# Kernel optimization log

Measured on AMD Instinct MI355X. Metric: run time of the kernel, lower is better.

## Reference

```python
import jax, jax.numpy as jnp
import numpy as np

DIM = 256
HEADS = 8
WS = 8
HID = 512
EPS = 1e-5

def _rel_index(ws):
    coords = np.arange(ws)
    grid = np.stack(np.meshgrid(coords, coords, indexing='ij')).reshape(2, -1)
    rel = (grid[:, :, None] - grid[:, None, :]).transpose(1, 2, 0)
    rel[:, :, 0] += ws - 1
    rel[:, :, 1] += ws - 1
    rel[:, :, 0] *= 2 * ws - 1
    return jnp.asarray(rel.sum(-1))  # [ws*ws, ws*ws] int

REL = _rel_index(WS)

def setup_inputs():
    key = jax.random.key(0)
    ks = iter(jax.random.split(key, 64))
    def w(shape, scale=0.02):
        return jax.random.normal(next(ks), shape, jnp.float32) * scale
    d = {}
    d['spatial'] = jax.random.normal(next(ks), (4, DIM, 128, 128), jnp.float32)
    d['frequency'] = jax.random.normal(next(ks), (4, DIM, 128, 128), jnp.float32)
    for p in ['s', 'f']:
        d[p + '_qw'] = w((DIM, DIM)); d[p + '_qb'] = jnp.zeros((DIM,), jnp.float32)
        d[p + '_kvw'] = w((2 * DIM, DIM)); d[p + '_kvb'] = jnp.zeros((2 * DIM,), jnp.float32)
        d[p + '_rpb'] = w(((2 * WS - 1) ** 2, HEADS))
        d[p + '_pw'] = w((DIM, DIM)); d[p + '_pb'] = jnp.zeros((DIM,), jnp.float32)
    for p in ['ns1', 'nfs', 'ns2', 'nf1', 'nsf', 'nf2']:
        d[p + '_g'] = jnp.ones((DIM,), jnp.float32); d[p + '_b'] = jnp.zeros((DIM,), jnp.float32)
    for p in ['ffns', 'ffnf']:
        d[p + '_w1'] = w((HID, DIM)); d[p + '_b1'] = jnp.zeros((HID,), jnp.float32)
        d[p + '_w2'] = w((DIM, HID)); d[p + '_b2'] = jnp.zeros((DIM,), jnp.float32)
    return d

def _ln(x, g, b):
    m = jnp.mean(x, -1, keepdims=True)
    v = jnp.mean((x - m) ** 2, -1, keepdims=True)
    return (x - m) / jnp.sqrt(v + EPS) * g + b

def _part(x):  # [B,C,H,W] -> [nW*B, WS*WS, C]
    B, C, H, W = x.shape
    x = x.transpose(0, 2, 3, 1).reshape(B, H // WS, WS, W // WS, WS, C)
    return x.transpose(0, 1, 3, 2, 4, 5).reshape(-1, WS * WS, C)

def _unpart(t, B, H, W):  # [nW*B, WS*WS, C] -> [B,C,H,W]
    C = t.shape[-1]
    x = t.reshape(B, H // WS, W // WS, WS, WS, C).transpose(0, 1, 3, 2, 4, 5).reshape(B, H, W, C)
    return x.transpose(0, 3, 1, 2)

def _xattn(qt, st, qw, qb, kvw, kvb, rpb, pw, pb):
    B_, N, C = qt.shape
    hd = C // HEADS
    q = (qt @ qw.T + qb).reshape(B_, N, HEADS, hd).transpose(0, 2, 1, 3) * (hd ** -0.5)
    kv = (st @ kvw.T + kvb).reshape(B_, N, 2, HEADS, hd).transpose(2, 0, 3, 1, 4)
    k, v = kv[0], kv[1]
    bias = rpb[REL.reshape(-1)].reshape(N, N, HEADS).transpose(2, 0, 1)  # [H,N,N]
    attn = jax.nn.softmax(jnp.einsum('bhnd,bhmd->bhnm', q, k) + bias[None], axis=-1)
    out = jnp.einsum('bhnm,bhmd->bhnd', attn, v).transpose(0, 2, 1, 3).reshape(B_, N, C)
    return out @ pw.T + pb

def _mlp(x, w1, b1, w2, b2):
    return jax.nn.gelu(x @ w1.T + b1, approximate=False) @ w2.T + b2

def _forward(spatial, frequency, s_qw, s_qb, s_kvw, s_kvb, s_rpb, s_pw, s_pb,
             f_qw, f_qb, f_kvw, f_kvb, f_rpb, f_pw, f_pb,
             ns1_g, ns1_b, nfs_g, nfs_b, ns2_g, ns2_b, nf1_g, nf1_b, nsf_g, nsf_b, nf2_g, nf2_b,
             ffns_w1, ffns_b1, ffns_w2, ffns_b2, ffnf_w1, ffnf_b1, ffnf_w2, ffnf_b2):
    B, C, H, W = spatial.shape
    s_win = _part(spatial)
    f_win = _part(frequency)
    # direction 1: spatial queries attend to frequency keys/values
    delta_s = _xattn(_ln(s_win, ns1_g, ns1_b), _ln(f_win, nfs_g, nfs_b),
                     s_qw, s_qb, s_kvw, s_kvb, s_rpb, s_pw, s_pb)
    s_win = s_win + delta_s
    s_win = s_win + _mlp(_ln(s_win, ns2_g, ns2_b), ffns_w1, ffns_b1, ffns_w2, ffns_b2)
    spatial_out = _unpart(s_win, B, H, W)
    # _part(spatial_out) == s_win exactly (partition/unpartition are inverses)
    # direction 2: frequency queries attend to updated spatial keys/values
    delta_f = _xattn(_ln(f_win, nf1_g, nf1_b), _ln(s_win, nsf_g, nsf_b),
                     f_qw, f_qb, f_kvw, f_kvb, f_rpb, f_pw, f_pb)
    f_win = f_win + delta_f
    f_win = f_win + _mlp(_ln(f_win, nf2_g, nf2_b), ffnf_w1, ffnf_b1, ffnf_w2, ffnf_b2)
    freq_out = _unpart(f_win, B, H, W)
    return spatial_out, freq_out

def reference(spatial, frequency, s_qw, s_qb, s_kvw, s_kvb, s_rpb, s_pw, s_pb,
              f_qw, f_qb, f_kvw, f_kvb, f_rpb, f_pw, f_pb,
              ns1_g, ns1_b, nfs_g, nfs_b, ns2_g, ns2_b, nf1_g, nf1_b, nsf_g, nsf_b, nf2_g, nf2_b,
              ffns_w1, ffns_b1, ffns_w2, ffns_b2, ffnf_w1, ffnf_b1, ffnf_w2, ffnf_b2):
    return _forward(spatial, frequency, s_qw, s_qb, s_kvw, s_kvb, s_rpb, s_pw, s_pb,
                    f_qw, f_qb, f_kvw, f_kvb, f_rpb, f_pw, f_pb,
                    ns1_g, ns1_b, nfs_g, nfs_b, ns2_g, ns2_b, nf1_g, nf1_b, nsf_g, nsf_b, nf2_g, nf2_b,
                    ffns_w1, ffns_b1, ffns_w2, ffns_b2, ffnf_w1, ffnf_b1, ffnf_w2, ffnf_b2)
```

## Files before the change

kernel.cpp:

```cpp
#include <hip/hip_runtime.h>

typedef unsigned short u16;
typedef unsigned int u32;
typedef unsigned long long u64;
using bf16x8 = __attribute__((ext_vector_type(8))) short;
using f32x4  = __attribute__((ext_vector_type(4))) float;
using u32x4  = __attribute__((ext_vector_type(4))) u32;
using u32x2  = __attribute__((ext_vector_type(2))) u32;

__device__ __forceinline__ float b2f(u16 h) {
    u32 u = ((u32)h) << 16;
    float f;
    __builtin_memcpy(&f, &u, 4);
    return f;
}
__device__ __forceinline__ u16 f2b(float f) {
    u32 u;
    __builtin_memcpy(&u, &f, 4);
    u32 r = (u + 0x7fffu + ((u >> 16) & 1u)) >> 16;
    return (u16)r;
}
__device__ __forceinline__ void gload16(const u16* g, u16* l) {
    __builtin_amdgcn_global_load_lds(
        (const __attribute__((address_space(1))) u32*)g,
        (__attribute__((address_space(3))) u32*)l, 16, 0, 0);
}

struct WPack { const float* s[10]; };

__global__ __launch_bounds__(256)
void wconv_kernel(WPack p, u16* __restrict__ dst) {
    const int id = blockIdx.x * 256 + threadIdx.x;
    const int e = id * 4;
    const int unit = e >> 16;
    const u64 arrmap = 0x9988766544332110ull;
    const u64 startmap = 0xECB9864310ull;
    const int arr = (int)((arrmap >> (unit * 4)) & 15);
    const int start = (int)((startmap >> (arr * 4)) & 15);
    const int off = e - (start << 16);
    f32x4 v = *(const f32x4*)(p.s[arr] + off);
    u32x2 w;
    w[0] = (u32)f2b(v[0]) | ((u32)f2b(v[1]) << 16);
    w[1] = (u32)f2b(v[2]) | ((u32)f2b(v[3]) << 16);
    *(u32x2*)(dst + e) = w;
}

__global__ __launch_bounds__(256)
void gather_ln_kernel(const float* __restrict__ X, const float* __restrict__ g,
                      const float* __restrict__ bta, u16* __restrict__ lno,
                      u16* __restrict__ raw) {
    __shared__ __align__(16) u16 win[128][264];
    __shared__ float mrs[128][2];
    const int tid = threadIdx.x;
    const int blk2 = blockIdx.x;
    const int b = blk2 >> 7, hb = (blk2 >> 3) & 15, wp = blk2 & 7;
#pragma unroll
    for (int it = 0; it < 8; ++it) {
        const int id = it * 256 + tid;
        const int c = id & 255, y = id >> 8;
        const size_t off =
            (((size_t)(b * 256 + c) * 128) + hb * 8 + y) * 128 + wp * 16;
        f32x4 v0 = *(const f32x4*)(X + off);
        f32x4 v1 = *(const f32x4*)(X + off + 4);
        f32x4 v2 = *(const f32x4*)(X + off + 8);
        f32x4 v3 = *(const f32x4*)(X + off + 12);
#pragma unroll
        for (int x = 0; x < 4; ++x) {
            win[y * 8 + x][c] = f2b(v0[x]);
            win[y * 8 + 4 + x][c] = f2b(v1[x]);
            win[64 + y * 8 + x][c] = f2b(v2[x]);
            win[64 + y * 8 + 4 + x][c] = f2b(v3[x]);
        }
    }
    __syncthreads();
    {
        const int tok = tid >> 1, half = tid & 1;
        float s = 0.f, s2 = 0.f;
#pragma unroll
        for (int i = 0; i < 16; ++i) {
            u32x4 rv = *(const u32x4*)&win[tok][half * 128 + i * 8];
            const u16* pv = (const u16*)&rv;
#pragma unroll
            for (int x = 0; x < 8; ++x) {
                float v = b2f(pv[x]);
                s += v;
                s2 += v * v;
            }
        }
        s += __shfl_xor(s, 1);
        s2 += __shfl_xor(s2, 1);
        const float mean = s * (1.f / 256.f);
        const float var = s2 * (1.f / 256.f) - mean * mean;
        if (!half) {
            mrs[tok][0] = mean;
            mrs[tok][1] = rsqrtf(var + 1e-5f);
        }
    }
    __syncthreads();
    const size_t base = (size_t)((b * 16 + hb) * 16 + wp * 2) * 64 * 256;
#pragma unroll
    for (int it = 0; it < 16; ++it) {
        const int e8 = it * 256 + tid;
        const int tok = e8 >> 5, c0 = (e8 & 31) * 8;
        u32x4 rv = *(const u32x4*)&win[tok][c0];
        if (raw) *(u32x4*)(raw + base + (size_t)e8 * 8) = rv;
        const u16* pv = (const u16*)&rv;
        const float mean = mrs[tok][0], rstd = mrs[tok][1];
        f32x4 g0 = *(const f32x4*)&g[c0];
        f32x4 g1 = *(const f32x4*)&g[c0 + 4];
        f32x4 t0 = *(const f32x4*)&bta[c0];
        f32x4 t1 = *(const f32x4*)&bta[c0 + 4];
        __align__(16) u16 outv[8];
#pragma unroll
        for (int x = 0; x < 4; ++x) {
            outv[x] = f2b((b2f(pv[x]) - mean) * rstd * g0[x] + t0[x]);
            outv[4 + x] = f2b((b2f(pv[4 + x]) - mean) * rstd * g1[x] + t1[x]);
        }
        *(u32x4*)(lno + base + (size_t)e8 * 8) = *(u32x4*)outv;
    }
}

__global__ __launch_bounds__(256)
void ln_kernel(const u16* __restrict__ X, const float* __restrict__ g,
               const float* __restrict__ bta, u16* __restrict__ Y) {
    const int wave = threadIdx.x >> 6, lane = threadIdx.x & 63;
    const size_t tok = (size_t)blockIdx.x * 4 + wave;
    const u16* x = X + tok * 256 + lane * 4;
    u32x2 v = *(const u32x2*)x;
    float f0 = b2f((u16)(v[0] & 0xffff)), f1 = b2f((u16)(v[0] >> 16));
    float f2v = b2f((u16)(v[1] & 0xffff)), f3 = b2f((u16)(v[1] >> 16));
    float s = f0 + f1 + f2v + f3;
    float s2 = f0 * f0 + f1 * f1 + f2v * f2v + f3 * f3;
#pragma unroll
    for (int off = 32; off; off >>= 1) {
        s += __shfl_xor(s, off);
        s2 += __shfl_xor(s2, off);
    }
    const float mean = s * (1.f / 256.f);
    const float var = s2 * (1.f / 256.f) - mean * mean;
    const float rstd = rsqrtf(var + 1e-5f);
    const int c = lane * 4;
    float o0 = (f0 - mean) * rstd * g[c + 0] + bta[c + 0];
    float o1 = (f1 - mean) * rstd * g[c + 1] + bta[c + 1];
    float o2 = (f2v - mean) * rstd * g[c + 2] + bta[c + 2];
    float o3 = (f3 - mean) * rstd * g[c + 3] + bta[c + 3];
    u32 w0 = (u32)f2b(o0) | ((u32)f2b(o1) << 16);
    u32 w1 = (u32)f2b(o2) | ((u32)f2b(o3) << 16);
    u32x2 w;
    w[0] = w0; w[1] = w1;
    *(u32x2*)(Y + tok * 256 + lane * 4) = w;
}

template <int K, int N, int RES, int EPI>
__global__ __launch_bounds__(256)
void gemm_kernel(const u16* __restrict__ A, const u16* __restrict__ Wt,
                 const float* __restrict__ bias, const u16* __restrict__ resw,
                 u16* __restrict__ Cout) {
    constexpr int S = N / 64;
    constexpr int NPH = K / 128;
    __shared__ __align__(16) u16 As[64][128];
    __shared__ __align__(16) u16 Bs[64][128];
    const int tid = threadIdx.x;
    const int lane = tid & 63, w = tid >> 6;
    const int cl = lane & 15, g = lane >> 4;
    const int wr = w >> 1, wc = w & 1;
    const int bid = blockIdx.x;
    const int xcd = bid & 7, rest = bid >> 3;
    const int strip = rest % S, mseq = rest / S;
    const int m0 = (xcd * 128 + mseq) * 64;
    const int n0 = strip * 64;
    const int srow = lane >> 4;
    const int sch = lane & 15;
    f32x4 acc[2][2] = {};
#pragma unroll
    for (int ph = 0; ph < NPH; ++ph) {
        if (ph) __syncthreads();
#pragma unroll
        for (int it = 0; it < 4; ++it) {
            const int rp = w * 16 + it * 4;
            const int row = rp + srow;
            const int ch = (sch & 8) | ((sch ^ row) & 7);
            gload16(&A[(size_t)(m0 + row) * K + ph * 128 + ch * 8], &As[rp][0]);
            gload16(&Wt[(size_t)(n0 + row) * K + ph * 128 + ch * 8], &Bs[rp][0]);
        }
        asm volatile("s_waitcnt vmcnt(0)" ::: "memory");
        __syncthreads();
#pragma unroll
        for (int ks = 0; ks < 4; ++ks) {
            const int J = ks * 4 + g;
            bf16x8 af[2], bw[2];
#pragma unroll
            for (int i = 0; i < 2; ++i) {
                const int r = wr * 32 + i * 16 + cl;
                af[i] = *(const bf16x8*)&As[r][((J & 8) | ((J ^ r) & 7)) * 8];
            }
#pragma unroll
            for (int j = 0; j < 2; ++j) {
                const int r = wc * 32 + j * 16 + cl;
                bw[j] = *(const bf16x8*)&Bs[r][((J & 8) | ((J ^ r) & 7)) * 8];
            }
#pragma unroll
            for (int i = 0; i < 2; ++i)
#pragma unroll
                for (int j = 0; j < 2; ++j)
                    acc[i][j] = __builtin_amdgcn_mfma_f32_16x16x32_bf16(
                        af[i], bw[j], acc[i][j], 0, 0, 0);
        }
    }
    __syncthreads();
    u16 (*Cs)[72] = (u16(*)[72])&As[0][0];
#pragma unroll
    for (int i = 0; i < 2; ++i)
#pragma unroll
        for (int j = 0; j < 2; ++j)
#pragma unroll
            for (int rr = 0; rr < 4; ++rr)
                Cs[wr * 32 + i * 16 + g * 4 + rr][wc * 32 + j * 16 + cl] =
                    f2b(acc[i][j][rr]);
    __syncthreads();
#pragma unroll
    for (int it = 0; it < 2; ++it) {
        const int idx = it * 256 + tid;
        const int row = idx >> 3, ch = idx & 7;
        const int grow = m0 + row, gcol = n0 + ch * 8;
        u32x4 cv = *(const u32x4*)&Cs[row][ch * 8];
        const u16* pc = (const u16*)&cv;
        f32x4 b0 = *(const f32x4*)&bias[gcol];
        f32x4 b1 = *(const f32x4*)&bias[gcol + 4];
        float v[8];
#pragma unroll
        for (int x = 0; x < 4; ++x) {
            v[x] = b2f(pc[x]) + b0[x];
            v[4 + x] = b2f(pc[4 + x]) + b1[x];
        }
        if constexpr (RES == 1) {
            u32x4 rv = *(const u32x4*)&resw[(size_t)grow * N + gcol];
            const u16* pr = (const u16*)&rv;
#pragma unroll
            for (int x = 0; x < 8; ++x) v[x] += b2f(pr[x]);
        }
        if constexpr (EPI == 1)
#pragma unroll
            for (int x = 0; x < 8; ++x)
                v[x] = 0.5f * v[x] * (1.f + erff(v[x] * 0.70710678118654752f));
        u32x4 ov;
#pragma unroll
        for (int x = 0; x < 4; ++x)
            ov[x] = (u32)f2b(v[2 * x]) | ((u32)f2b(v[2 * x + 1]) << 16);
        *(u32x4*)&Cout[(size_t)grow * N + gcol] = ov;
    }
}

__global__ __launch_bounds__(256)
void attn_mfma_kernel(const u16* __restrict__ Q, const u16* __restrict__ KV,
                      const float* __restrict__ rpb, u16* __restrict__ O) {
    __shared__ __align__(16) u16 Pq[4][64][72];
    __shared__ __align__(16) u16 Vt[4][32][72];
    __shared__ float rb[4][228];
    const int w = threadIdx.x >> 6, lane = threadIdx.x & 63;
    const int gw = blockIdx.x * 4 + w;
    const int win = gw >> 3, h = gw & 7;
    const int c = lane & 15, g = lane >> 4;
    for (int i = lane; i < 225; i += 64) rb[w][i] = rpb[i * 8 + h];
    {
        const u16* Vrow = KV + ((size_t)(win * 64 + lane)) * 512 + 256 + h * 32;
        u32x4 vv[4];
#pragma unroll
        for (int ch = 0; ch < 4; ++ch) vv[ch] = *(const u32x4*)(Vrow + ch * 8);
        const u16* pv = (const u16*)vv;
#pragma unroll
        for (int d = 0; d < 32; ++d) Vt[w][d][lane] = pv[d];
    }
    const u16* Qb = Q + ((size_t)win * 64 + c) * 256 + h * 32 + g * 8;
    const u16* Kb = KV + ((size_t)win * 64 + c) * 512 + h * 32 + g * 8;
    bf16x8 qf[4], kf[4];
#pragma unroll
    for (int t = 0; t < 4; ++t) {
        qf[t] = *(const bf16x8*)(Qb + (size_t)t * 16 * 256);
        kf[t] = *(const bf16x8*)(Kb + (size_t)t * 16 * 512);
    }
    f32x4 st[4][4];
#pragma unroll
    for (int kb = 0; kb < 4; ++kb)
#pragma unroll
        for (int qb = 0; qb < 4; ++qb) {
            f32x4 z = {0.f, 0.f, 0.f, 0.f};
            st[kb][qb] = __builtin_amdgcn_mfma_f32_16x16x32_bf16(kf[kb], qf[qb], z, 0, 0, 0);
        }
    __syncthreads();
    const float scale = 0.17677669529663687f;
    const int qy2 = c >> 3, qx = c & 7;
#pragma unroll
    for (int qb = 0; qb < 4; ++qb) {
        float sv[16];
#pragma unroll
        for (int kb = 0; kb < 4; ++kb)
#pragma unroll
            for (int r = 0; r < 4; ++r) {
                const int k = kb * 16 + 4 * g + r;
                const int dy = (qb * 2 + qy2) - (k >> 3) + 7;
                const int dx = qx - (k & 7) + 7;
                sv[kb * 4 + r] = st[kb][qb][r] * scale + rb[w][dy * 15 + dx];
            }
        float mx = sv[0];
#pragma unroll
        for (int j = 1; j < 16; ++j) mx = fmaxf(mx, sv[j]);
        mx = fmaxf(mx, __shfl_xor(mx, 16));
        mx = fmaxf(mx, __shfl_xor(mx, 32));
        float sum = 0.f;
#pragma unroll
        for (int j = 0; j < 16; ++j) {
            sv[j] = __expf(sv[j] - mx);
            sum += sv[j];
        }
        sum += __shfl_xor(sum, 16);
        sum += __shfl_xor(sum, 32);
        const float inv = 1.f / sum;
#pragma unroll
        for (int kb = 0; kb < 4; ++kb) {
            u32x2 pk;
            pk[0] = (u32)f2b(sv[kb * 4 + 0] * inv) | ((u32)f2b(sv[kb * 4 + 1] * inv) << 16);
            pk[1] = (u32)f2b(sv[kb * 4 + 2] * inv) | ((u32)f2b(sv[kb * 4 + 3] * inv) << 16);
            *(u32x2*)&Pq[w][qb * 16 + c][kb * 16 + 4 * g] = pk;
        }
    }
    __syncthreads();
    f32x4 ot[4][2] = {};
#pragma unroll
    for (int ks = 0; ks < 2; ++ks) {
        bf16x8 bfr[2];
#pragma unroll
        for (int db = 0; db < 2; ++db)
            bfr[db] = *(const bf16x8*)&Vt[w][db * 16 + c][ks * 32 + g * 8];
#pragma unroll
        for (int qb = 0; qb < 4; ++qb) {
            bf16x8 af = *(const bf16x8*)&Pq[w][qb * 16 + c][ks * 32 + g * 8];
#pragma unroll
            for (int db = 0; db < 2; ++db)
                ot[qb][db] = __builtin_amdgcn_mfma_f32_16x16x32_bf16(af, bfr[db], ot[qb][db], 0, 0, 0);
        }
    }
    u16* Ob = O + ((size_t)win * 64) * 256 + h * 32;
#pragma unroll
    for (int qb = 0; qb < 4; ++qb)
#pragma unroll
        for (int db = 0; db < 2; ++db)
#pragma unroll
            for (int r = 0; r < 4; ++r)
                Ob[(size_t)(qb * 16 + 4 * g + r) * 256 + db * 16 + c] = f2b(ot[qb][db][r]);
}

__global__ __launch_bounds__(256)
void scatter_kernel(const u16* __restrict__ Wn, float* __restrict__ out) {
    __shared__ __align__(16) u16 win[128][264];
    const int tid = threadIdx.x;
    const int blk2 = blockIdx.x;
    const int b = blk2 >> 7, hb = (blk2 >> 3) & 15, wp = blk2 & 7;
    const size_t base = (size_t)((b * 16 + hb) * 16 + wp * 2) * 64 * 256;
#pragma unroll
    for (int it = 0; it < 16; ++it) {
        const int e8 = it * 256 + tid;
        const int tok = e8 >> 5, c0 = (e8 & 31) * 8;
        *(u32x4*)&win[tok][c0] = *(const u32x4*)(Wn + base + (size_t)e8 * 8);
    }
    __syncthreads();
#pragma unroll
    for (int it = 0; it < 8; ++it) {
        const int id = it * 256 + tid;
        const int c = id & 255, y = id >> 8;
        f32x4 o0, o1, o2, o3;
#pragma unroll
        for (int x = 0; x < 4; ++x) {
            o0[x] = b2f(win[y * 8 + x][c]);
            o1[x] = b2f(win[y * 8 + 4 + x][c]);
            o2[x] = b2f(win[64 + y * 8 + x][c]);
            o3[x] = b2f(win[64 + y * 8 + 4 + x][c]);
        }
        const size_t oo =
            (((size_t)(b * 256 + c) * 128) + hb * 8 + y) * 128 + wp * 16;
        *(f32x4*)(out + oo) = o0;
        *(f32x4*)(out + oo + 4) = o1;
        *(f32x4*)(out + oo + 8) = o2;
        *(f32x4*)(out + oo + 12) = o3;
    }
}

extern "C" void kernel_launch(void* const* d_in, const int* in_sizes, int n_in,
                              void* d_out, int out_size, void* d_ws,
                              size_t ws_size, hipStream_t stream) {
    const float* spatial = (const float*)d_in[0];
    const float* freq    = (const float*)d_in[1];
    const float* s_qw  = (const float*)d_in[2];
    const float* s_qb  = (const float*)d_in[3];
    const float* s_kvw = (const float*)d_in[4];
    const float* s_kvb = (const float*)d_in[5];
    const float* s_rpb = (const float*)d_in[6];
    const float* s_pw  = (const float*)d_in[7];
    const float* s_pb  = (const float*)d_in[8];
    const float* f_qw  = (const float*)d_in[9];
    const float* f_qb  = (const float*)d_in[10];
    const float* f_kvw = (const float*)d_in[11];
    const float* f_kvb = (const float*)d_in[12];
    const float* f_rpb = (const float*)d_in[13];
    const float* f_pw  = (const float*)d_in[14];
    const float* f_pb  = (const float*)d_in[15];
    const float* ns1_g = (const float*)d_in[16];
    const float* ns1_b = (const float*)d_in[17];
    const float* nfs_g = (const float*)d_in[18];
    const float* nfs_b = (const float*)d_in[19];
    const float* ns2_g = (const float*)d_in[20];
    const float* ns2_b = (const float*)d_in[21];
    const float* nf1_g = (const float*)d_in[22];
    const float* nf1_b = (const float*)d_in[23];
    const float* nsf_g = (const float*)d_in[24];
    const float* nsf_b = (const float*)d_in[25];
    const float* nf2_g = (const float*)d_in[26];
    const float* nf2_b = (const float*)d_in[27];
    const float* ffns_w1 = (const float*)d_in[28];
    const float* ffns_b1 = (const float*)d_in[29];
    const float* ffns_w2 = (const float*)d_in[30];
    const float* ffns_b2 = (const float*)d_in[31];
    const float* ffnf_w1 = (const float*)d_in[32];
    const float* ffnf_b1 = (const float*)d_in[33];
    const float* ffnf_w2 = (const float*)d_in[34];
    const float* ffnf_b2 = (const float*)d_in[35];

    float* out = (float*)d_out;
    char* ob = (char*)d_out;
    char* ws = (char*)d_ws;
    const size_t MB32 = (size_t)32 << 20;
    u16* U0  = (u16*)ob;
    u16* U1  = (u16*)(ob + MB32);
    u16* U23 = (u16*)(ob + 2 * MB32);
    u16* W0  = (u16*)ws;
    u16* W1  = (u16*)(ws + MB32);
    u16* WB  = (u16*)(ws + 2 * MB32);
    u16* R0  = (u16*)(ws + 2 * MB32 + (2 << 20));
    u16* R1  = (u16*)(ws + 2 * MB32 + (2 << 20) + MB32);

    const u16* w_sq  = WB;
    const u16* w_skv = WB + 1 * 65536;
    const u16* w_sp  = WB + 3 * 65536;
    const u16* w_sw1 = WB + 4 * 65536;
    const u16* w_sw2 = WB + 6 * 65536;
    const u16* w_fq  = WB + 8 * 65536;
    const u16* w_fkv = WB + 9 * 65536;
    const u16* w_fp  = WB + 11 * 65536;
    const u16* w_fw1 = WB + 12 * 65536;
    const u16* w_fw2 = WB + 14 * 65536;

    WPack wp;
    wp.s[0] = s_qw;  wp.s[1] = s_kvw; wp.s[2] = s_pw;  wp.s[3] = ffns_w1;
    wp.s[4] = ffns_w2; wp.s[5] = f_qw; wp.s[6] = f_kvw; wp.s[7] = f_pw;
    wp.s[8] = ffnf_w1; wp.s[9] = ffnf_w2;

    const dim3 B(256);
    wconv_kernel<<<1024, B, 0, stream>>>(wp, WB);
    gather_ln_kernel<<<512, B, 0, stream>>>(spatial, ns1_g, ns1_b, U0, R0);
    gather_ln_kernel<<<512, B, 0, stream>>>(freq, nfs_g, nfs_b, U1, R1);
    gemm_kernel<256, 512, 0, 0><<<8192, B, 0, stream>>>(
        U1, w_skv, s_kvb, nullptr, U23);
    gemm_kernel<256, 256, 0, 0><<<4096, B, 0, stream>>>(
        U0, w_sq, s_qb, nullptr, U1);
    attn_mfma_kernel<<<2048, B, 0, stream>>>(U1, U23, s_rpb, U0);
    gemm_kernel<256, 256, 1, 0><<<4096, B, 0, stream>>>(
        U0, w_sp, s_pb, R0, U1);
    ln_kernel<<<16384, B, 0, stream>>>(U1, ns2_g, ns2_b, U0);
    gemm_kernel<256, 512, 0, 1><<<8192, B, 0, stream>>>(
        U0, w_sw1, ffns_b1, nullptr, U23);
    gemm_kernel<512, 256, 1, 0><<<4096, B, 0, stream>>>(
        U23, w_sw2, ffns_b2, U1, W0);
    ln_kernel<<<16384, B, 0, stream>>>(W0, nsf_g, nsf_b, U0);
    gemm_kernel<256, 512, 0, 0><<<8192, B, 0, stream>>>(
        U0, w_fkv, f_kvb, nullptr, U23);
    gather_ln_kernel<<<512, B, 0, stream>>>(freq, nf1_g, nf1_b, U0, nullptr);
    gemm_kernel<256, 256, 0, 0><<<4096, B, 0, stream>>>(
        U0, w_fq, f_qb, nullptr, U1);
    attn_mfma_kernel<<<2048, B, 0, stream>>>(U1, U23, f_rpb, U0);
    gemm_kernel<256, 256, 1, 0><<<4096, B, 0, stream>>>(
        U0, w_fp, f_pb, R1, W1);
    ln_kernel<<<16384, B, 0, stream>>>(W1, nf2_g, nf2_b, U0);
    gemm_kernel<256, 512, 0, 1><<<8192, B, 0, stream>>>(
        U0, w_fw1, ffnf_b1, nullptr, U23);
    scatter_kernel<<<512, B, 0, stream>>>(W0, out);
    gemm_kernel<512, 256, 1, 0><<<4096, B, 0, stream>>>(
        U23, w_fw2, ffnf_b2, W1, W0);
    scatter_kernel<<<512, B, 0, stream>>>(W0, out + 16777216);
}
```

Baseline: 599.4 us.

## Fuse LayerNorm into GEMM A-tile prologue, drop standalone LN kernels

LayerNorm now runs inside the GEMM kernels. Each block loads the full 64x256 A tile into shared memory, computes per-token mean and rstd, and normalises the tile in place before the MFMA loop. This removes the separate ln_kernel launches, the third gather_ln pass and the extra normalized-activation round trips through global memory. The cost is that every N-strip block repeats the LN math, the A tile in shared memory doubles in size, and the LN phase adds a barrier before the matmul, which may hurt occupancy.

```diff
diff --git a/kernel.cpp b/kernel.cpp
--- a/kernel.cpp
+++ b/kernel.cpp
@@ -46,11 +46,8 @@
 }
 
 __global__ __launch_bounds__(256)
-void gather_ln_kernel(const float* __restrict__ X, const float* __restrict__ g,
-                      const float* __restrict__ bta, u16* __restrict__ lno,
-                      u16* __restrict__ raw) {
+void gather_raw_kernel(const float* __restrict__ X, u16* __restrict__ raw) {
     __shared__ __align__(16) u16 win[128][264];
-    __shared__ float mrs[128][2];
     const int tid = threadIdx.x;
     const int blk2 = blockIdx.x;
     const int b = blk2 >> 7, hb = (blk2 >> 3) & 15, wp = blk2 & 7;
@@ -73,92 +70,25 @@
         }
     }
     __syncthreads();
-    {
-        const int tok = tid >> 1, half = tid & 1;
-        float s = 0.f, s2 = 0.f;
-#pragma unroll
-        for (int i = 0; i < 16; ++i) {
-            u32x4 rv = *(const u32x4*)&win[tok][half * 128 + i * 8];
-            const u16* pv = (const u16*)&rv;
-#pragma unroll
-            for (int x = 0; x < 8; ++x) {
-                float v = b2f(pv[x]);
-                s += v;
-                s2 += v * v;
-            }
-        }
-        s += __shfl_xor(s, 1);
-        s2 += __shfl_xor(s2, 1);
-        const float mean = s * (1.f / 256.f);
-        const float var = s2 * (1.f / 256.f) - mean * mean;
-        if (!half) {
-            mrs[tok][0] = mean;
-            mrs[tok][1] = rsqrtf(var + 1e-5f);
-        }
-    }
-    __syncthreads();
     const size_t base = (size_t)((b * 16 + hb) * 16 + wp * 2) * 64 * 256;
 #pragma unroll
     for (int it = 0; it < 16; ++it) {
         const int e8 = it * 256 + tid;
         const int tok = e8 >> 5, c0 = (e8 & 31) * 8;
-        u32x4 rv = *(const u32x4*)&win[tok][c0];
-        if (raw) *(u32x4*)(raw + base + (size_t)e8 * 8) = rv;
-        const u16* pv = (const u16*)&rv;
-        const float mean = mrs[tok][0], rstd = mrs[tok][1];
-        f32x4 g0 = *(const f32x4*)&g[c0];
-        f32x4 g1 = *(const f32x4*)&g[c0 + 4];
-        f32x4 t0 = *(const f32x4*)&bta[c0];
-        f32x4 t1 = *(const f32x4*)&bta[c0 + 4];
-        __align__(16) u16 outv[8];
-#pragma unroll
-        for (int x = 0; x < 4; ++x) {
-            outv[x] = f2b((b2f(pv[x]) - mean) * rstd * g0[x] + t0[x]);
-            outv[4 + x] = f2b((b2f(pv[4 + x]) - mean) * rstd * g1[x] + t1[x]);
-        }
-        *(u32x4*)(lno + base + (size_t)e8 * 8) = *(u32x4*)outv;
-    }
-}
-
-__global__ __launch_bounds__(256)
-void ln_kernel(const u16* __restrict__ X, const float* __restrict__ g,
-               const float* __restrict__ bta, u16* __restrict__ Y) {
-    const int wave = threadIdx.x >> 6, lane = threadIdx.x & 63;
-    const size_t tok = (size_t)blockIdx.x * 4 + wave;
-    const u16* x = X + tok * 256 + lane * 4;
-    u32x2 v = *(const u32x2*)x;
-    float f0 = b2f((u16)(v[0] & 0xffff)), f1 = b2f((u16)(v[0] >> 16));
-    float f2v = b2f((u16)(v[1] & 0xffff)), f3 = b2f((u16)(v[1] >> 16));
-    float s = f0 + f1 + f2v + f3;
-    float s2 = f0 * f0 + f1 * f1 + f2v * f2v + f3 * f3;
-#pragma unroll
-    for (int off = 32; off; off >>= 1) {
-        s += __shfl_xor(s, off);
-        s2 += __shfl_xor(s2, off);
-    }
-    const float mean = s * (1.f / 256.f);
-    const float var = s2 * (1.f / 256.f) - mean * mean;
-    const float rstd = rsqrtf(var + 1e-5f);
-    const int c = lane * 4;
-    float o0 = (f0 - mean) * rstd * g[c + 0] + bta[c + 0];
-    float o1 = (f1 - mean) * rstd * g[c + 1] + bta[c + 1];
-    float o2 = (f2v - mean) * rstd * g[c + 2] + bta[c + 2];
-    float o3 = (f3 - mean) * rstd * g[c + 3] + bta[c + 3];
-    u32 w0 = (u32)f2b(o0) | ((u32)f2b(o1) << 16);
-    u32 w1 = (u32)f2b(o2) | ((u32)f2b(o3) << 16);
-    u32x2 w;
-    w[0] = w0; w[1] = w1;
-    *(u32x2*)(Y + tok * 256 + lane * 4) = w;
-}
-
-template <int K, int N, int RES, int EPI>
+        *(u32x4*)(raw + base + (size_t)e8 * 8) = *(const u32x4*)&win[tok][c0];
+    }
+}
+
+template <int K, int N, int LNA, int RES, int EPI>
 __global__ __launch_bounds__(256)
 void gemm_kernel(const u16* __restrict__ A, const u16* __restrict__ Wt,
-                 const float* __restrict__ bias, const u16* __restrict__ resw,
+                 const float* __restrict__ bias, const float* __restrict__ lng,
+                 const float* __restrict__ lnb, const u16* __restrict__ resw,
                  u16* __restrict__ Cout) {
+    static_assert(!LNA || K == 256, "LN fusion requires K=256");
     constexpr int S = N / 64;
-    constexpr int NPH = K / 128;
-    __shared__ __align__(16) u16 As[64][128];
+    constexpr int AK = LNA ? 256 : 128;
+    __shared__ __align__(16) u16 As[64][AK];
     __shared__ __align__(16) u16 Bs[64][128];
     const int tid = threadIdx.x;
     const int lane = tid & 63, w = tid >> 6;
@@ -169,42 +99,153 @@
     const int strip = rest % S, mseq = rest / S;
     const int m0 = (xcd * 128 + mseq) * 64;
     const int n0 = strip * 64;
-    const int srow = lane >> 4;
-    const int sch = lane & 15;
     f32x4 acc[2][2] = {};
-#pragma unroll
-    for (int ph = 0; ph < NPH; ++ph) {
-        if (ph) __syncthreads();
-#pragma unroll
-        for (int it = 0; it < 4; ++it) {
-            const int rp = w * 16 + it * 4;
-            const int row = rp + srow;
-            const int ch = (sch & 8) | ((sch ^ row) & 7);
-            gload16(&A[(size_t)(m0 + row) * K + ph * 128 + ch * 8], &As[rp][0]);
-            gload16(&Wt[(size_t)(n0 + row) * K + ph * 128 + ch * 8], &Bs[rp][0]);
+
+    if constexpr (LNA) {
+        {
+            const int row2 = lane >> 5, sc32 = lane & 31;
+#pragma unroll
+            for (int it = 0; it < 8; ++it) {
+                const int rp = w * 16 + it * 2;
+                const int row = rp + row2;
+                const int ch = (sc32 & 24) | ((sc32 ^ row) & 7);
+                gload16(&A[(size_t)(m0 + row) * K + ch * 8], &As[rp][0]);
+            }
+            const int row4 = lane >> 4, sc16 = lane & 15;
+#pragma unroll
+            for (int it = 0; it < 4; ++it) {
+                const int rp = w * 16 + it * 4;
+                const int row = rp + row4;
+                const int ch = (sc16 & 8) | ((sc16 ^ row) & 7);
+                gload16(&Wt[(size_t)(n0 + row) * K + ch * 8], &Bs[rp][0]);
+            }
         }
         asm volatile("s_waitcnt vmcnt(0)" ::: "memory");
         __syncthreads();
-#pragma unroll
-        for (int ks = 0; ks < 4; ++ks) {
-            const int J = ks * 4 + g;
-            bf16x8 af[2], bw[2];
-#pragma unroll
-            for (int i = 0; i < 2; ++i) {
-                const int r = wr * 32 + i * 16 + cl;
-                af[i] = *(const bf16x8*)&As[r][((J & 8) | ((J ^ r) & 7)) * 8];
-            }
-#pragma unroll
-            for (int j = 0; j < 2; ++j) {
-                const int r = wc * 32 + j * 16 + cl;
-                bw[j] = *(const bf16x8*)&Bs[r][((J & 8) | ((J ^ r) & 7)) * 8];
-            }
-#pragma unroll
-            for (int i = 0; i < 2; ++i)
-#pragma unroll
-                for (int j = 0; j < 2; ++j)
-                    acc[i][j] = __builtin_amdgcn_mfma_f32_16x16x32_bf16(
-                        af[i], bw[j], acc[i][j], 0, 0, 0);
+        {
+            const int tok = tid >> 2, qd = tid & 3;
+            u32x4 cv[8];
+            float s = 0.f, s2 = 0.f;
+#pragma unroll
+            for (int i = 0; i < 8; ++i) {
+                const int ch = qd * 8 + i;
+                const int a = (ch & 24) | ((ch ^ tok) & 7);
+                cv[i] = *(const u32x4*)&As[tok][a * 8];
+                const u16* pv = (const u16*)&cv[i];
+#pragma unroll
+                for (int x = 0; x < 8; ++x) {
+                    float v = b2f(pv[x]);
+                    s += v;
+                    s2 += v * v;
+                }
+            }
+            s += __shfl_xor(s, 1);  s += __shfl_xor(s, 2);
+            s2 += __shfl_xor(s2, 1); s2 += __shfl_xor(s2, 2);
+            const float mean = s * (1.f / 256.f);
+            const float var = s2 * (1.f / 256.f) - mean * mean;
+            const float rstd = rsqrtf(var + 1e-5f);
+#pragma unroll
+            for (int i = 0; i < 8; ++i) {
+                const int ch = qd * 8 + i;
+                const int a = (ch & 24) | ((ch ^ tok) & 7);
+                const u16* pv = (const u16*)&cv[i];
+                f32x4 g0 = *(const f32x4*)&lng[ch * 8];
+                f32x4 g1 = *(const f32x4*)&lng[ch * 8 + 4];
+                f32x4 t0 = *(const f32x4*)&lnb[ch * 8];
+                f32x4 t1 = *(const f32x4*)&lnb[ch * 8 + 4];
+                __align__(16) u16 ov[8];
+#pragma unroll
+                for (int x = 0; x < 4; ++x) {
+                    ov[x] = f2b((b2f(pv[x]) - mean) * rstd * g0[x] + t0[x]);
+                    ov[4 + x] =
+                        f2b((b2f(pv[4 + x]) - mean) * rstd * g1[x] + t1[x]);
+                }
+                *(u32x4*)&As[tok][a * 8] = *(u32x4*)ov;
+            }
+        }
+        __syncthreads();
+#pragma unroll
+        for (int ph = 0; ph < 2; ++ph) {
+            if (ph) {
+                __syncthreads();
+                const int row4 = lane >> 4, sc16 = lane & 15;
+#pragma unroll
+                for (int it = 0; it < 4; ++it) {
+                    const int rp = w * 16 + it * 4;
+                    const int row = rp + row4;
+                    const int ch = (sc16 & 8) | ((sc16 ^ row) & 7);
+                    gload16(&Wt[(size_t)(n0 + row) * K + 128 + ch * 8],
+                            &Bs[rp][0]);
+                }
+                asm volatile("s_waitcnt vmcnt(0)" ::: "memory");
+                __syncthreads();
+            }
+#pragma unroll
+            for (int ks = 0; ks < 4; ++ks) {
+                const int J16 = ks * 4 + g;
+                const int JA = ph * 16 + J16;
+                bf16x8 af[2], bw[2];
+#pragma unroll
+                for (int i = 0; i < 2; ++i) {
+                    const int r = wr * 32 + i * 16 + cl;
+                    af[i] = *(const bf16x8*)
+                        &As[r][(((JA & 24) | ((JA ^ r) & 7))) * 8];
+                }
+#pragma unroll
+                for (int j = 0; j < 2; ++j) {
+                    const int r = wc * 32 + j * 16 + cl;
+                    bw[j] = *(const bf16x8*)
+                        &Bs[r][(((J16 & 8) | ((J16 ^ r) & 7))) * 8];
+                }
+#pragma unroll
+                for (int i = 0; i < 2; ++i)
+#pragma unroll
+                    for (int j = 0; j < 2; ++j)
+                        acc[i][j] = __builtin_amdgcn_mfma_f32_16x16x32_bf16(
+                            af[i], bw[j], acc[i][j], 0, 0, 0);
+            }
+        }
+    } else {
+        constexpr int NPH = K / 128;
+        const int srow = lane >> 4, sch = lane & 15;
+#pragma unroll
+        for (int ph = 0; ph < NPH; ++ph) {
+            if (ph) __syncthreads();
+#pragma unroll
+            for (int it = 0; it < 4; ++it) {
+                const int rp = w * 16 + it * 4;
+                const int row = rp + srow;
+                const int ch = (sch & 8) | ((sch ^ row) & 7);
+                gload16(&A[(size_t)(m0 + row) * K + ph * 128 + ch * 8],
+                        &As[rp][0]);
+                gload16(&Wt[(size_t)(n0 + row) * K + ph * 128 + ch * 8],
+                        &Bs[rp][0]);
+            }
+            asm volatile("s_waitcnt vmcnt(0)" ::: "memory");
+            __syncthreads();
+#pragma unroll
+            for (int ks = 0; ks < 4; ++ks) {
+                const int J = ks * 4 + g;
+                bf16x8 af[2], bw[2];
+#pragma unroll
+                for (int i = 0; i < 2; ++i) {
+                    const int r = wr * 32 + i * 16 + cl;
+                    af[i] = *(const bf16x8*)
+                        &As[r][(((J & 8) | ((J ^ r) & 7))) * 8];
+                }
+#pragma unroll
+                for (int j = 0; j < 2; ++j) {
+                    const int r = wc * 32 + j * 16 + cl;
+                    bw[j] = *(const bf16x8*)
+                        &Bs[r][(((J & 8) | ((J ^ r) & 7))) * 8];
+                }
+#pragma unroll
+                for (int i = 0; i < 2; ++i)
+#pragma unroll
+                    for (int j = 0; j < 2; ++j)
+                        acc[i][j] = __builtin_amdgcn_mfma_f32_16x16x32_bf16(
+                            af[i], bw[j], acc[i][j], 0, 0, 0);
+            }
         }
     }
     __syncthreads();
@@ -456,34 +497,30 @@
 
     const dim3 B(256);
     wconv_kernel<<<1024, B, 0, stream>>>(wp, WB);
-    gather_ln_kernel<<<512, B, 0, stream>>>(spatial, ns1_g, ns1_b, U0, R0);
-    gather_ln_kernel<<<512, B, 0, stream>>>(freq, nfs_g, nfs_b, U1, R1);
-    gemm_kernel<256, 512, 0, 0><<<8192, B, 0, stream>>>(
-        U1, w_skv, s_kvb, nullptr, U23);
-    gemm_kernel<256, 256, 0, 0><<<4096, B, 0, stream>>>(
-        U0, w_sq, s_qb, nullptr, U1);
+    gather_raw_kernel<<<512, B, 0, stream>>>(spatial, R0);
+    gather_raw_kernel<<<512, B, 0, stream>>>(freq, R1);
+    gemm_kernel<256, 512, 1, 0, 0><<<8192, B, 0, stream>>>(
+        R1, w_skv, s_kvb, nfs_g, nfs_b, nullptr, U23);
+    gemm_kernel<256, 256, 1, 0, 0><<<4096, B, 0, stream>>>(
+        R0, w_sq, s_qb, ns1_g, ns1_b, nullptr, U1);
     attn_mfma_kernel<<<2048, B, 0, stream>>>(U1, U23, s_rpb, U0);
-    gemm_kernel<256, 256, 1, 0><<<4096, B, 0, stream>>>(
-        U0, w_sp, s_pb, R0, U1);
-    ln_kernel<<<16384, B, 0, stream>>>(U1, ns2_g, ns2_b, U0);
-    gemm_kernel<256, 512, 0, 1><<<8192, B, 0, stream>>>(
-        U0, w_sw1, ffns_b1, nullptr, U23);
-    gemm_kernel<512, 256, 1, 0><<<4096, B, 0, stream>>>(
-        U23, w_sw2, ffns_b2, U1, W0);
-    ln_kernel<<<16384, B, 0, stream>>>(W0, nsf_g, nsf_b, U0);
-    gemm_kernel<256, 512, 0, 0><<<8192, B, 0, stream>>>(
-        U0, w_fkv, f_kvb, nullptr, U23);
-    gather_ln_kernel<<<512, B, 0, stream>>>(freq, nf1_g, nf1_b, U0, nullptr);
-    gemm_kernel<256, 256, 0, 0><<<4096, B, 0, stream>>>(
-        U0, w_fq, f_qb, nullptr, U1);
+    gemm_kernel<256, 256, 0, 1, 0><<<4096, B, 0, stream>>>(
+        U0, w_sp, s_pb, nullptr, nullptr, R0, U1);
+    gemm_kernel<256, 512, 1, 0, 1><<<8192, B, 0, stream>>>(
+        U1, w_sw1, ffns_b1, ns2_g, ns2_b, nullptr, U23);
+    gemm_kernel<512, 256, 0, 1, 0><<<4096, B, 0, stream>>>(
+        U23, w_sw2, ffns_b2, nullptr, nullptr, U1, W0);
+    gemm_kernel<256, 512, 1, 0, 0><<<8192, B, 0, stream>>>(
+        W0, w_fkv, f_kvb, nsf_g, nsf_b, nullptr, U23);
+    gemm_kernel<256, 256, 1, 0, 0><<<4096, B, 0, stream>>>(
+        R1, w_fq, f_qb, nf1_g, nf1_b, nullptr, U1);
     attn_mfma_kernel<<<2048, B, 0, stream>>>(U1, U23, f_rpb, U0);
-    gemm_kernel<256, 256, 1, 0><<<4096, B, 0, stream>>>(
-        U0, w_fp, f_pb, R1, W1);
-    ln_kernel<<<16384, B, 0, stream>>>(W1, nf2_g, nf2_b, U0);
-    gemm_kernel<256, 512, 0, 1><<<8192, B, 0, stream>>>(
-        U0, w_fw1, ffnf_b1, nullptr, U23);
+    gemm_kernel<256, 256, 0, 1, 0><<<4096, B, 0, stream>>>(
+        U0, w_fp, f_pb, nullptr, nullptr, R1, W1);
+    gemm_kernel<256, 512, 1, 0, 1><<<8192, B, 0, stream>>>(
+        W1, w_fw1, ffnf_b1, nf2_g, nf2_b, nullptr, U23);
     scatter_kernel<<<512, B, 0, stream>>>(W0, out);
-    gemm_kernel<512, 256, 1, 0><<<4096, B, 0, stream>>>(
-        U23, w_fw2, ffnf_b2, W1, W0);
+    gemm_kernel<512, 256, 0, 1, 0><<<4096, B, 0, stream>>>(
+        U23, w_fw2, ffnf_b2, nullptr, nullptr, W1, W0);
     scatter_kernel<<<512, B, 0, stream>>>(W0, out + 16777216);
 }
```

Measured after the change: 1.132 ms. 88.8% more time.

## Double-buffer GEMM K-loop with 64-wide chunks and reuse residual for nf1 LayerNorm

Applied to the files above, without the earlier changes.

The GEMM kernel now splits K into 64-wide chunks held in two LDS buffers. The next chunk is prefetched with global_load_lds while the current one is consumed, using partial vmcnt waits and explicit barriers in place of a full drain per phase. Separately, the nf1 LayerNorm now reads the already gathered bf16 residual R1 through ln_kernel, instead of gathering the fp32 frequency tensor again. The pipelining adds barriers per chunk and halves the MFMA work between them, and the LN change assumes R1 still holds the original windowed frequency at that point.

```diff
diff --git a/kernel.cpp b/kernel.cpp
--- a/kernel.cpp
+++ b/kernel.cpp
@@ -24,6 +24,13 @@
     __builtin_amdgcn_global_load_lds(
         (const __attribute__((address_space(1))) u32*)g,
         (__attribute__((address_space(3))) u32*)l, 16, 0, 0);
+}
+__device__ __forceinline__ void hard_barrier() {
+    asm volatile("" ::: "memory");
+    __builtin_amdgcn_sched_barrier(0);
+    __builtin_amdgcn_s_barrier();
+    __builtin_amdgcn_sched_barrier(0);
+    asm volatile("" ::: "memory");
 }
 
 struct WPack { const float* s[10]; };
@@ -157,9 +164,9 @@
                  const float* __restrict__ bias, const u16* __restrict__ resw,
                  u16* __restrict__ Cout) {
     constexpr int S = N / 64;
-    constexpr int NPH = K / 128;
-    __shared__ __align__(16) u16 As[64][128];
-    __shared__ __align__(16) u16 Bs[64][128];
+    constexpr int NPH = K / 64;
+    __shared__ __align__(16) u16 As[2][64 * 64];
+    __shared__ __align__(16) u16 Bs[2][64 * 64];
     const int tid = threadIdx.x;
     const int lane = tid & 63, w = tid >> 6;
     const int cl = lane & 15, g = lane >> 4;
@@ -169,35 +176,47 @@
     const int strip = rest % S, mseq = rest / S;
     const int m0 = (xcd * 128 + mseq) * 64;
     const int n0 = strip * 64;
-    const int srow = lane >> 4;
-    const int sch = lane & 15;
+    const int rowg = lane >> 3;
+    const int sch = lane & 7;
     f32x4 acc[2][2] = {};
-#pragma unroll
-    for (int ph = 0; ph < NPH; ++ph) {
-        if (ph) __syncthreads();
-#pragma unroll
-        for (int it = 0; it < 4; ++it) {
-            const int rp = w * 16 + it * 4;
-            const int row = rp + srow;
-            const int ch = (sch & 8) | ((sch ^ row) & 7);
-            gload16(&A[(size_t)(m0 + row) * K + ph * 128 + ch * 8], &As[rp][0]);
-            gload16(&Wt[(size_t)(n0 + row) * K + ph * 128 + ch * 8], &Bs[rp][0]);
-        }
-        asm volatile("s_waitcnt vmcnt(0)" ::: "memory");
-        __syncthreads();
-#pragma unroll
-        for (int ks = 0; ks < 4; ++ks) {
+
+    auto stage = [&](int c) {
+        const int buf = c & 1;
+#pragma unroll
+        for (int it = 0; it < 2; ++it) {
+            const int rp = w * 16 + it * 8;
+            const int row = rp + rowg;
+            const int ch = sch ^ (row & 7);
+            gload16(&A[(size_t)(m0 + row) * K + c * 64 + ch * 8],
+                    &As[buf][rp * 64]);
+            gload16(&Wt[(size_t)(n0 + row) * K + c * 64 + ch * 8],
+                    &Bs[buf][rp * 64]);
+        }
+    };
+    stage(0);
+    stage(1);
+#pragma unroll
+    for (int c = 0; c < NPH; ++c) {
+        if (c + 1 < NPH)
+            asm volatile("s_waitcnt vmcnt(4)" ::: "memory");
+        else
+            asm volatile("s_waitcnt vmcnt(0)" ::: "memory");
+        hard_barrier();
+        const u16* Ab = &As[c & 1][0];
+        const u16* Bb = &Bs[c & 1][0];
+#pragma unroll
+        for (int ks = 0; ks < 2; ++ks) {
             const int J = ks * 4 + g;
             bf16x8 af[2], bw[2];
 #pragma unroll
             for (int i = 0; i < 2; ++i) {
                 const int r = wr * 32 + i * 16 + cl;
-                af[i] = *(const bf16x8*)&As[r][((J & 8) | ((J ^ r) & 7)) * 8];
+                af[i] = *(const bf16x8*)(Ab + r * 64 + (J ^ (r & 7)) * 8);
             }
 #pragma unroll
             for (int j = 0; j < 2; ++j) {
                 const int r = wc * 32 + j * 16 + cl;
-                bw[j] = *(const bf16x8*)&Bs[r][((J & 8) | ((J ^ r) & 7)) * 8];
+                bw[j] = *(const bf16x8*)(Bb + r * 64 + (J ^ (r & 7)) * 8);
             }
 #pragma unroll
             for (int i = 0; i < 2; ++i)
@@ -206,8 +225,10 @@
                     acc[i][j] = __builtin_amdgcn_mfma_f32_16x16x32_bf16(
                         af[i], bw[j], acc[i][j], 0, 0, 0);
         }
-    }
-    __syncthreads();
+        asm volatile("s_waitcnt lgkmcnt(0)" ::: "memory");
+        hard_barrier();
+        if (c + 2 < NPH) stage(c + 2);
+    }
     u16 (*Cs)[72] = (u16(*)[72])&As[0][0];
 #pragma unroll
     for (int i = 0; i < 2; ++i)
@@ -473,7 +494,7 @@
     ln_kernel<<<16384, B, 0, stream>>>(W0, nsf_g, nsf_b, U0);
     gemm_kernel<256, 512, 0, 0><<<8192, B, 0, stream>>>(
         U0, w_fkv, f_kvb, nullptr, U23);
-    gather_ln_kernel<<<512, B, 0, stream>>>(freq, nf1_g, nf1_b, U0, nullptr);
+    ln_kernel<<<16384, B, 0, stream>>>(R1, nf1_g, nf1_b, U0);
     gemm_kernel<256, 256, 0, 0><<<4096, B, 0, stream>>>(
         U0, w_fq, f_qb, nullptr, U1);
     attn_mfma_kernel<<<2048, B, 0, stream>>>(U1, U23, f_rpb, U0);
```

Measured after the change: 584.0 us. -2.6%, faster.
